# Kernel optimization log

Hardware: AMD Instinct MI355X
Metric: run time of the kernel (lower is better)

Reference implementation:

```python
import jax, jax.numpy as jnp
import numpy as np

BATCH, DIM, DB_SIZE, TOP_K = 2048, 512, 50000, 5

def setup_inputs() -> dict:
    key = jax.random.key(0)
    k1, k2 = jax.random.split(key)
    h_current = jax.random.normal(k1, (BATCH, DIM), dtype=jnp.float32)
    history_db = jax.random.normal(k2, (DB_SIZE, DIM), dtype=jnp.float32) * 0.01
    alpha = jnp.float32(0.5)
    return {"h_current": h_current, "history_db": history_db, "alpha": alpha, "top_k": TOP_K}

def _l2_normalize(x, eps=1e-12):
    # matches F.normalize(p=2): x / max(||x||, eps)
    n = jnp.linalg.norm(x, axis=-1, keepdims=True)
    return x / jnp.maximum(n, eps)

def reference(h_current, history_db, alpha, top_k):
    h_norm = _l2_normalize(h_current)            # (B, D)
    db_norm = _l2_normalize(history_db)          # (M, D)
    similarity = h_norm @ db_norm.T              # (B, M)
    topk_sim, topk_idx = jax.lax.top_k(similarity, top_k)  # (B, K)
    mu = jax.nn.softmax(topk_sim, axis=-1)       # (B, K)
    topk_embeddings = history_db[topk_idx]       # (B, K, D)
    h_retrieved = jnp.einsum('bk,bkd->bd', mu, topk_embeddings)
    a = jax.nn.sigmoid(alpha)
    return a * h_current + (1.0 - a) * h_retrieved
```

## Files before the change

### kernel.cpp

```cpp
#include <hip/hip_runtime.h>

#define BATCH   2048
#define DIM     512
#define DB_N    50000
#define TOPK    5
#define PADN    50176
#define NCHUNK  56
#define CTILES  7
#define CCOLS   896
#define TM      128
#define TN      128
#define NFIN    12

typedef float f32x4 __attribute__((ext_vector_type(4)));
typedef long long i64;

__device__ __forceinline__ void async16(const void* g, void* l) {
    __builtin_amdgcn_global_load_lds(
        (const __attribute__((address_space(1))) unsigned int*)g,
        (__attribute__((address_space(3))) unsigned int*)l, 16, 0, 0);
}

__device__ __forceinline__ unsigned sortbits(float v) {
    const int u = __float_as_int(v);
    return (unsigned)(u ^ ((u >> 31) | 0x80000000));
}

template<int NROWS>
__global__ void convert_kernel(const float* __restrict__ src, unsigned char* __restrict__ dst,
                               float* __restrict__ invp, int nreal) {
    const int r    = blockIdx.x * 4 + (threadIdx.x >> 6);
    const int lane = threadIdx.x & 63;
    float4 a = {0,0,0,0}, b = {0,0,0,0};
    float ss = 0.f;
    if (r < nreal) {
        const float* row = src + (size_t)r * DIM;
        a = *(const float4*)(row + lane * 8);
        b = *(const float4*)(row + lane * 8 + 4);
        ss = a.x*a.x + a.y*a.y + a.z*a.z + a.w*a.w
           + b.x*b.x + b.y*b.y + b.z*b.z + b.w*b.w;
    }
    #pragma unroll
    for (int off = 1; off < 64; off <<= 1) ss += __shfl_xor(ss, off);
    const float inv = 1.0f / fmaxf(sqrtf(ss), 1e-12f);
    const float s16 = inv * 16.0f;
    int lo = __builtin_amdgcn_cvt_pk_fp8_f32(a.x * s16, a.y * s16, 0, false);
    lo     = __builtin_amdgcn_cvt_pk_fp8_f32(a.z * s16, a.w * s16, lo, true);
    int hi = __builtin_amdgcn_cvt_pk_fp8_f32(b.x * s16, b.y * s16, 0, false);
    hi     = __builtin_amdgcn_cvt_pk_fp8_f32(b.z * s16, b.w * s16, hi, true);
    const int kb = lane >> 4;
    const int w  = (lane >> 1) & 7;
    int2 u2; u2.x = lo; u2.y = hi;
    *(int2*)(dst + ((size_t)kb * NROWS + r) * 128 + ((w ^ (r & 7)) << 4) + ((lane & 1) << 3)) = u2;
    if (invp && lane == 0) invp[r] = inv;
}

__global__ __launch_bounds__(512, 4) void sim_topk_kernel(
    const unsigned char* __restrict__ hzf, const unsigned char* __restrict__ dbzf,
    unsigned* __restrict__ pc) {

    __shared__ __align__(16) unsigned char As[2][TM * 128];
    __shared__ __align__(16) unsigned char Bs[2][TN * 128];
    __shared__ unsigned mrg[2][4][64][TOPK];

    const int tid  = threadIdx.x;
    const int lane = tid & 63;
    const int l15  = lane & 15;
    const int lhi  = lane >> 4;
    const int wid  = tid >> 6;
    const int uw   = __builtin_amdgcn_readfirstlane(wid);
    const int wm   = wid >> 2;
    const int wn   = wid & 3;
    const int mc   = blockIdx.x % NCHUNK;
    const int rb   = blockIdx.x / NCHUNK;
    const int c0   = mc * CCOLS;

    unsigned k0[16], k1[16];
    #pragma unroll
    for (int q = 0; q < 16; ++q) { k0[q] = 0u; k1[q] = 0u; }

    auto STAGE = [&](int buf, int t, int kb) {
        const unsigned char* ga = hzf +
            (((size_t)kb * BATCH + (size_t)rb * TM) * 8 + uw * 128 + lane) * 16;
        const unsigned char* gb = dbzf +
            (((size_t)kb * PADN + (size_t)(c0 + t * TN)) * 8 + uw * 128 + lane) * 16;
        async16(ga,        &As[buf][uw * 2048]);
        async16(ga + 1024, &As[buf][uw * 2048 + 1024]);
        async16(gb,        &Bs[buf][uw * 2048]);
        async16(gb + 1024, &Bs[buf][uw * 2048 + 1024]);
    };

    f32x4 acc[4][2];

    STAGE(0, 0, 0);

    int p = 0;
    #pragma unroll 1
    for (int t = 0; t < CTILES; ++t) {
        #pragma unroll
        for (int mf = 0; mf < 4; ++mf)
            #pragma unroll
            for (int nf = 0; nf < 2; ++nf) acc[mf][nf] = (f32x4){0.f, 0.f, 0.f, 0.f};

        #pragma unroll
        for (int kb = 0; kb < 4; ++kb) {
            const int np = p + 1;
            if (np < CTILES * 4) {
                STAGE(np & 1, np >> 2, np & 3);
                asm volatile("s_waitcnt vmcnt(4)" ::: "memory");
            } else {
                asm volatile("s_waitcnt vmcnt(0)" ::: "memory");
            }
            __builtin_amdgcn_s_barrier();
            __builtin_amdgcn_sched_barrier(0);

            const unsigned char* ta = As[p & 1];
            const unsigned char* tb = Bs[p & 1];
            #pragma unroll
            for (int ks = 0; ks < 4; ++ks) {
                const int sub = ks * 2 + (lhi >> 1);
                const int c8  = (lhi & 1) << 3;
                i64 af[4], bfr[2];
                #pragma unroll
                for (int mf = 0; mf < 4; ++mf) {
                    const int r = wm * 64 + mf * 16 + l15;
                    af[mf] = *(const i64*)(ta + r * 128 + ((sub ^ (r & 7)) << 4) + c8);
                }
                #pragma unroll
                for (int nf = 0; nf < 2; ++nf) {
                    const int r = wn * 32 + nf * 16 + l15;
                    bfr[nf] = *(const i64*)(tb + r * 128 + ((sub ^ (r & 7)) << 4) + c8);
                }
                __builtin_amdgcn_s_setprio(1);
                #pragma unroll
                for (int mf = 0; mf < 4; ++mf)
                    #pragma unroll
                    for (int nf = 0; nf < 2; ++nf)
                        acc[mf][nf] = __builtin_amdgcn_mfma_f32_16x16x32_fp8_fp8(
                            af[mf], bfr[nf], acc[mf][nf], 0, 0, 0);
                __builtin_amdgcn_s_setprio(0);
            }
            __builtin_amdgcn_sched_barrier(0);
            __builtin_amdgcn_s_barrier();
            ++p;
        }

        const int tc = c0 + t * TN;
        #pragma unroll
        for (int nf = 0; nf < 2; ++nf) {
            const int  gcol  = tc + wn * 32 + nf * 16 + l15;
            const bool valid = gcol < DB_N;
            #pragma unroll
            for (int mf = 0; mf < 4; ++mf)
                #pragma unroll
                for (int i = 0; i < 4; ++i) {
                    const int q = mf * 4 + i;
                    const unsigned key = valid
                        ? ((sortbits(acc[mf][nf][i]) & 0xFFFF0000u) | (unsigned)gcol) : 0u;
                    const unsigned hi2 = key > k0[q] ? key   : k0[q];
                    const unsigned lo2 = key > k0[q] ? k0[q] : key;
                    k1[q] = lo2 > k1[q] ? lo2 : k1[q];
                    k0[q] = hi2;
                }
        }
    }

    #pragma unroll
    for (int mf = 0; mf < 4; ++mf)
        #pragma unroll
        for (int i = 0; i < 4; ++i) {
            const int q = mf * 4 + i;
            unsigned a0 = k0[q], a1 = k1[q];
            #pragma unroll
            for (int it = 0; it < TOPK; ++it) {
                unsigned w = a0;
                #pragma unroll
                for (int sh = 1; sh < 16; sh <<= 1) {
                    const unsigned o = (unsigned)__shfl_xor((int)w, sh);
                    w = o > w ? o : w;
                }
                const bool own = (a0 == w) && (w != 0u);
                a0 = own ? a1 : a0;
                a1 = own ? 0u : a1;
                if (l15 == q) mrg[wm][wn][mf * 16 + lhi * 4 + i][it] = w;
            }
        }
    __syncthreads();

    if (wn == 0) {
        unsigned bv[TOPK] = {0u, 0u, 0u, 0u, 0u};
        #pragma unroll
        for (int qq = 0; qq < 4; ++qq)
            #pragma unroll
            for (int j = 0; j < TOPK; ++j) {
                const unsigned u = mrg[wm][qq][lane][j];
                #pragma unroll
                for (int k = TOPK - 1; k >= 1; --k) {
                    const bool gt  = u > bv[k];
                    const bool gtp = u > bv[k - 1];
                    bv[k] = gt ? (gtp ? bv[k - 1] : u) : bv[k];
                }
                if (u > bv[0]) bv[0] = u;
            }
        const int row = rb * TM + wm * 64 + lane;
        #pragma unroll
        for (int j = 0; j < TOPK; ++j)
            pc[((size_t)row * NCHUNK + mc) * TOPK + j] = bv[j];
    }
}

__global__ void finalize_kernel(const float* __restrict__ h, const float* __restrict__ db,
                                const float* __restrict__ alpha_p,
                                const unsigned* __restrict__ pc,
                                const float* __restrict__ inv_db,
                                float* __restrict__ out) {
    const int b    = blockIdx.x;
    const int tid  = threadIdx.x;
    const int lane = tid & 63;
    const int wv   = tid >> 6;
    const int NC   = NCHUNK * TOPK;

    __shared__ int   fid[NFIN];
    __shared__ float fsim[NFIN];
    __shared__ float invh_s;
    __shared__ float mu_s[TOPK];
    __shared__ int   id_s[TOPK];

    if (wv == 0) {
        const unsigned* cp = pc + (size_t)b * NC;
        unsigned v[5];
        #pragma unroll
        for (int j = 0; j < 5; ++j) {
            const int c = lane + j * 64;
            v[j] = (c < NC) ? cp[c] : 0u;
        }
        for (int it = 0; it < NFIN; ++it) {
            unsigned m = v[0];
            #pragma unroll
            for (int j = 1; j < 5; ++j) m = v[j] > m ? v[j] : m;
            #pragma unroll
            for (int sh = 1; sh < 64; sh <<= 1) {
                const unsigned o = (unsigned)__shfl_xor((int)m, sh);
                m = o > m ? o : m;
            }
            if (lane == 0) {
                int gi = (int)(m & 0xFFFFu);
                fid[it] = gi < DB_N ? gi : DB_N - 1;
            }
            #pragma unroll
            for (int j = 0; j < 5; ++j) if (v[j] == m) v[j] = 0u;
        }
    } else if (wv == 1) {
        const float* hr = h + (size_t)b * DIM;
        const float4 a = *(const float4*)(hr + lane * 8);
        const float4 c = *(const float4*)(hr + lane * 8 + 4);
        float ss = a.x*a.x + a.y*a.y + a.z*a.z + a.w*a.w
                 + c.x*c.x + c.y*c.y + c.z*c.z + c.w*c.w;
        #pragma unroll
        for (int off = 1; off < 64; off <<= 1) ss += __shfl_xor(ss, off);
        if (lane == 0) invh_s = 1.0f / fmaxf(sqrtf(ss), 1e-12f);
    }
    __syncthreads();

    const float* hr = h + (size_t)b * DIM;
    for (int f = wv; f < NFIN; f += 4) {
        const int gi = fid[f];
        const float* dr = db + (size_t)gi * DIM;
        const float4 ha = *(const float4*)(hr + lane * 8);
        const float4 hb = *(const float4*)(hr + lane * 8 + 4);
        const float4 da = *(const float4*)(dr + lane * 8);
        const float4 dc = *(const float4*)(dr + lane * 8 + 4);
        float d = ha.x*da.x + ha.y*da.y + ha.z*da.z + ha.w*da.w
                + hb.x*dc.x + hb.y*dc.y + hb.z*dc.z + hb.w*dc.w;
        #pragma unroll
        for (int off = 1; off < 64; off <<= 1) d += __shfl_xor(d, off);
        if (lane == 0) fsim[f] = d * invh_s * inv_db[gi];
    }
    __syncthreads();

    if (tid == 0) {
        bool used[NFIN];
        #pragma unroll
        for (int j = 0; j < NFIN; ++j) used[j] = false;
        float bv[TOPK]; int bi[TOPK];
        for (int it = 0; it < TOPK; ++it) {
            float m = -3.0e38f; int mj = 0, mi = 0x7fffffff;
            for (int j = 0; j < NFIN; ++j) {
                if (used[j]) continue;
                if (fsim[j] > m || (fsim[j] == m && fid[j] < mi)) {
                    m = fsim[j]; mj = j; mi = fid[j];
                }
            }
            used[mj] = true; bv[it] = m; bi[it] = mi;
        }
        float ssum = 0.f, w[TOPK];
        #pragma unroll
        for (int j = 0; j < TOPK; ++j) { w[j] = expf(bv[j] - bv[0]); ssum += w[j]; }
        #pragma unroll
        for (int j = 0; j < TOPK; ++j) { mu_s[j] = w[j] / ssum; id_s[j] = bi[j]; }
    }
    __syncthreads();

    const float a = 1.0f / (1.0f + expf(-alpha_p[0]));
    for (int d = tid; d < DIM; d += 256) {
        float r = 0.f;
        #pragma unroll
        for (int j = 0; j < TOPK; ++j) r += mu_s[j] * db[(size_t)id_s[j] * DIM + d];
        out[(size_t)b * DIM + d] = a * h[(size_t)b * DIM + d] + (1.f - a) * r;
    }
}

extern "C" void kernel_launch(void* const* d_in, const int* in_sizes, int n_in,
                              void* d_out, int out_size, void* d_ws, size_t ws_size,
                              hipStream_t stream) {
    const float* h     = (const float*)d_in[0];
    const float* db    = (const float*)d_in[1];
    const float* alpha = (const float*)d_in[2];
    float* out = (float*)d_out;

    const size_t dbzf_bytes = (size_t)PADN * DIM;
    const size_t hzf_bytes  = (size_t)BATCH * DIM;
    const size_t inv_bytes  = (size_t)PADN * 4;

    unsigned char* dbzf  = (unsigned char*)d_ws;
    unsigned char* hzf   = (unsigned char*)d_ws + dbzf_bytes;
    float*         invdb = (float*)((char*)d_ws + dbzf_bytes + hzf_bytes);
    unsigned*      pc    = (unsigned*)((char*)d_ws + dbzf_bytes + hzf_bytes + inv_bytes);

    convert_kernel<PADN><<<PADN / 4, 256, 0, stream>>>(db, dbzf, invdb, DB_N);
    convert_kernel<BATCH><<<BATCH / 4, 256, 0, stream>>>(h, hzf, nullptr, BATCH);
    sim_topk_kernel<<<16 * NCHUNK, 512, 0, stream>>>(hzf, dbzf, pc);
    finalize_kernel<<<BATCH, 256, 0, stream>>>(h, db, alpha, pc, invdb, out);
}
```

Measured before the change: 177.8 us.

## Enlarge similarity GEMM tile to 256x128 with triple-buffered LDS pipeline

Rewrites the fp8 similarity+top-k kernel to use 256x128 block tiles with 8 waves each computing a 64x64 sub-tile, and triple-buffers LDS loads two stages ahead instead of double buffering. MFMA work is split into four quadrant groups with explicit LDS fragment loads between them. Column chunks double (28 chunks of 1792 columns), halving the grid and the per-row partial candidate count that the finalize kernel scans. This raises arithmetic intensity and cuts redundant A/B traffic, at the cost of higher register and LDS use, occupancy limited to one block per CU, and only 224 blocks for 256 CUs.

New measurement: 192.9 us. 8.5% more time.

```diff
diff --git a/kernel.cpp b/kernel.cpp
--- a/kernel.cpp
+++ b/kernel.cpp
@@ -5,11 +5,12 @@
 #define DB_N    50000
 #define TOPK    5
 #define PADN    50176
-#define NCHUNK  56
-#define CTILES  7
-#define CCOLS   896
-#define TM      128
-#define TN      128
+#define NCHUNK  28
+#define CTILES  14
+#define CCOLS   1792
+#define KSTEPS  56
+#define BM      256
+#define BN      128
 #define NFIN    12
 
 typedef float f32x4 __attribute__((ext_vector_type(4)));
@@ -55,22 +56,21 @@
     if (invp && lane == 0) invp[r] = inv;
 }
 
-__global__ __launch_bounds__(512, 4) void sim_topk_kernel(
+__global__ __launch_bounds__(512, 1) void sim_topk_kernel(
     const unsigned char* __restrict__ hzf, const unsigned char* __restrict__ dbzf,
     unsigned* __restrict__ pc) {
 
-    __shared__ __align__(16) unsigned char As[2][TM * 128];
-    __shared__ __align__(16) unsigned char Bs[2][TN * 128];
-    __shared__ unsigned mrg[2][4][64][TOPK];
+    __shared__ __align__(16) unsigned char As[3][BM * 128];
+    __shared__ __align__(16) unsigned char Bs[3][BN * 128];
+    __shared__ unsigned mrg[4][2][64][TOPK];
 
     const int tid  = threadIdx.x;
     const int lane = tid & 63;
     const int l15  = lane & 15;
     const int lhi  = lane >> 4;
     const int wid  = tid >> 6;
-    const int uw   = __builtin_amdgcn_readfirstlane(wid);
-    const int wm   = wid >> 2;
-    const int wn   = wid & 3;
+    const int wm   = wid >> 1;
+    const int wn   = wid & 1;
     const int mc   = blockIdx.x % NCHUNK;
     const int rb   = blockIdx.x / NCHUNK;
     const int c0   = mc * CCOLS;
@@ -79,89 +79,146 @@
     #pragma unroll
     for (int q = 0; q < 16; ++q) { k0[q] = 0u; k1[q] = 0u; }
 
-    auto STAGE = [&](int buf, int t, int kb) {
-        const unsigned char* ga = hzf +
-            (((size_t)kb * BATCH + (size_t)rb * TM) * 8 + uw * 128 + lane) * 16;
-        const unsigned char* gb = dbzf +
-            (((size_t)kb * PADN + (size_t)(c0 + t * TN)) * 8 + uw * 128 + lane) * 16;
-        async16(ga,        &As[buf][uw * 2048]);
-        async16(ga + 1024, &As[buf][uw * 2048 + 1024]);
-        async16(gb,        &Bs[buf][uw * 2048]);
-        async16(gb + 1024, &Bs[buf][uw * 2048 + 1024]);
+    auto STAGE = [&](int s) {
+        const int buf = s % 3;
+        const int kb  = s & 3;
+        const int t   = s >> 2;
+        const unsigned char* ga = hzf + ((size_t)kb * BATCH + (size_t)rb * BM) * 128;
+        const unsigned char* gb = dbzf + ((size_t)kb * PADN + (size_t)(c0 + t * BN)) * 128;
+        #pragma unroll
+        for (int j = 0; j < 4; ++j)
+            async16(ga + tid * 16 + j * 8192, &As[buf][tid * 16 + j * 8192]);
+        #pragma unroll
+        for (int j = 0; j < 2; ++j)
+            async16(gb + tid * 16 + j * 8192, &Bs[buf][tid * 16 + j * 8192]);
     };
 
-    f32x4 acc[4][2];
-
-    STAGE(0, 0, 0);
-
-    int p = 0;
+    const int s2 = lhi >> 1;
+    const int c8 = (lhi & 1) << 3;
+
+    f32x4 acc[4][4];
+    #pragma unroll
+    for (int mf = 0; mf < 4; ++mf)
+        #pragma unroll
+        for (int nf = 0; nf < 4; ++nf) acc[mf][nf] = (f32x4){0.f, 0.f, 0.f, 0.f};
+
+    STAGE(0);
+    STAGE(1);
+
     #pragma unroll 1
-    for (int t = 0; t < CTILES; ++t) {
-        #pragma unroll
-        for (int mf = 0; mf < 4; ++mf)
-            #pragma unroll
-            for (int nf = 0; nf < 2; ++nf) acc[mf][nf] = (f32x4){0.f, 0.f, 0.f, 0.f};
-
-        #pragma unroll
-        for (int kb = 0; kb < 4; ++kb) {
-            const int np = p + 1;
-            if (np < CTILES * 4) {
-                STAGE(np & 1, np >> 2, np & 3);
-                asm volatile("s_waitcnt vmcnt(4)" ::: "memory");
-            } else {
-                asm volatile("s_waitcnt vmcnt(0)" ::: "memory");
-            }
-            __builtin_amdgcn_s_barrier();
-            __builtin_amdgcn_sched_barrier(0);
-
-            const unsigned char* ta = As[p & 1];
-            const unsigned char* tb = Bs[p & 1];
+    for (int s = 0; s < KSTEPS; ++s) {
+        if (s == KSTEPS - 1) { asm volatile("s_waitcnt vmcnt(0)" ::: "memory"); }
+        else                 { asm volatile("s_waitcnt vmcnt(6)" ::: "memory"); }
+        __builtin_amdgcn_s_barrier();
+        __builtin_amdgcn_sched_barrier(0);
+        if (s + 2 < KSTEPS) STAGE(s + 2);
+
+        const unsigned char* ta = As[s % 3];
+        const unsigned char* tb = Bs[s % 3];
+
+        i64 a0[8], a1[8], b0[8], b1[8];
+        #pragma unroll
+        for (int mf = 0; mf < 2; ++mf)
             #pragma unroll
             for (int ks = 0; ks < 4; ++ks) {
-                const int sub = ks * 2 + (lhi >> 1);
-                const int c8  = (lhi & 1) << 3;
-                i64 af[4], bfr[2];
-                #pragma unroll
-                for (int mf = 0; mf < 4; ++mf) {
-                    const int r = wm * 64 + mf * 16 + l15;
-                    af[mf] = *(const i64*)(ta + r * 128 + ((sub ^ (r & 7)) << 4) + c8);
-                }
-                #pragma unroll
-                for (int nf = 0; nf < 2; ++nf) {
-                    const int r = wn * 32 + nf * 16 + l15;
-                    bfr[nf] = *(const i64*)(tb + r * 128 + ((sub ^ (r & 7)) << 4) + c8);
-                }
-                __builtin_amdgcn_s_setprio(1);
+                const int r = wm * 64 + mf * 16 + l15;
+                a0[mf * 4 + ks] = *(const i64*)(ta + r * 128 + (((ks * 2 + s2) ^ (r & 7)) << 4) + c8);
+            }
+        #pragma unroll
+        for (int nf = 0; nf < 2; ++nf)
+            #pragma unroll
+            for (int ks = 0; ks < 4; ++ks) {
+                const int r = wn * 64 + nf * 16 + l15;
+                b0[nf * 4 + ks] = *(const i64*)(tb + r * 128 + (((ks * 2 + s2) ^ (r & 7)) << 4) + c8);
+            }
+        asm volatile("s_waitcnt lgkmcnt(0)" ::: "memory");
+        __builtin_amdgcn_sched_barrier(0);
+        __builtin_amdgcn_s_setprio(1);
+        #pragma unroll
+        for (int mf = 0; mf < 2; ++mf)
+            #pragma unroll
+            for (int nf = 0; nf < 2; ++nf)
+                #pragma unroll
+                for (int ks = 0; ks < 4; ++ks)
+                    acc[mf][nf] = __builtin_amdgcn_mfma_f32_16x16x32_fp8_fp8(
+                        a0[mf * 4 + ks], b0[nf * 4 + ks], acc[mf][nf], 0, 0, 0);
+        __builtin_amdgcn_s_setprio(0);
+        __builtin_amdgcn_sched_barrier(0);
+
+        #pragma unroll
+        for (int nf = 0; nf < 2; ++nf)
+            #pragma unroll
+            for (int ks = 0; ks < 4; ++ks) {
+                const int r = wn * 64 + (nf + 2) * 16 + l15;
+                b1[nf * 4 + ks] = *(const i64*)(tb + r * 128 + (((ks * 2 + s2) ^ (r & 7)) << 4) + c8);
+            }
+        asm volatile("s_waitcnt lgkmcnt(0)" ::: "memory");
+        __builtin_amdgcn_sched_barrier(0);
+        __builtin_amdgcn_s_setprio(1);
+        #pragma unroll
+        for (int mf = 0; mf < 2; ++mf)
+            #pragma unroll
+            for (int nf = 0; nf < 2; ++nf)
+                #pragma unroll
+                for (int ks = 0; ks < 4; ++ks)
+                    acc[mf][nf + 2] = __builtin_amdgcn_mfma_f32_16x16x32_fp8_fp8(
+                        a0[mf * 4 + ks], b1[nf * 4 + ks], acc[mf][nf + 2], 0, 0, 0);
+        __builtin_amdgcn_s_setprio(0);
+        __builtin_amdgcn_sched_barrier(0);
+
+        #pragma unroll
+        for (int mf = 0; mf < 2; ++mf)
+            #pragma unroll
+            for (int ks = 0; ks < 4; ++ks) {
+                const int r = wm * 64 + (mf + 2) * 16 + l15;
+                a1[mf * 4 + ks] = *(const i64*)(ta + r * 128 + (((ks * 2 + s2) ^ (r & 7)) << 4) + c8);
+            }
+        asm volatile("s_waitcnt lgkmcnt(0)" ::: "memory");
+        __builtin_amdgcn_sched_barrier(0);
+        __builtin_amdgcn_s_setprio(1);
+        #pragma unroll
+        for (int mf = 0; mf < 2; ++mf)
+            #pragma unroll
+            for (int nf = 0; nf < 2; ++nf)
+                #pragma unroll
+                for (int ks = 0; ks < 4; ++ks)
+                    acc[mf + 2][nf + 2] = __builtin_amdgcn_mfma_f32_16x16x32_fp8_fp8(
+                        a1[mf * 4 + ks], b1[nf * 4 + ks], acc[mf + 2][nf + 2], 0, 0, 0);
+        __builtin_amdgcn_s_setprio(0);
+        __builtin_amdgcn_sched_barrier(0);
+
+        __builtin_amdgcn_s_setprio(1);
+        #pragma unroll
+        for (int mf = 0; mf < 2; ++mf)
+            #pragma unroll
+            for (int nf = 0; nf < 2; ++nf)
+                #pragma unroll
+                for (int ks = 0; ks < 4; ++ks)
+                    acc[mf + 2][nf] = __builtin_amdgcn_mfma_f32_16x16x32_fp8_fp8(
+                        a1[mf * 4 + ks], b0[nf * 4 + ks], acc[mf + 2][nf], 0, 0, 0);
+        __builtin_amdgcn_s_setprio(0);
+        __builtin_amdgcn_sched_barrier(0);
+
+        if ((s & 3) == 3) {
+            const int tc = c0 + (s >> 2) * BN;
+            #pragma unroll
+            for (int nf = 0; nf < 4; ++nf) {
+                const int  gcol  = tc + wn * 64 + nf * 16 + l15;
+                const bool valid = gcol < DB_N;
                 #pragma unroll
                 for (int mf = 0; mf < 4; ++mf)
                     #pragma unroll
-                    for (int nf = 0; nf < 2; ++nf)
-                        acc[mf][nf] = __builtin_amdgcn_mfma_f32_16x16x32_fp8_fp8(
-                            af[mf], bfr[nf], acc[mf][nf], 0, 0, 0);
-                __builtin_amdgcn_s_setprio(0);
-            }
-            __builtin_amdgcn_sched_barrier(0);
-            __builtin_amdgcn_s_barrier();
-            ++p;
-        }
-
-        const int tc = c0 + t * TN;
-        #pragma unroll
-        for (int nf = 0; nf < 2; ++nf) {
-            const int  gcol  = tc + wn * 32 + nf * 16 + l15;
-            const bool valid = gcol < DB_N;
-            #pragma unroll
-            for (int mf = 0; mf < 4; ++mf)
-                #pragma unroll
-                for (int i = 0; i < 4; ++i) {
-                    const int q = mf * 4 + i;
-                    const unsigned key = valid
-                        ? ((sortbits(acc[mf][nf][i]) & 0xFFFF0000u) | (unsigned)gcol) : 0u;
-                    const unsigned hi2 = key > k0[q] ? key   : k0[q];
-                    const unsigned lo2 = key > k0[q] ? k0[q] : key;
-                    k1[q] = lo2 > k1[q] ? lo2 : k1[q];
-                    k0[q] = hi2;
-                }
+                    for (int i = 0; i < 4; ++i) {
+                        const int q = mf * 4 + i;
+                        const unsigned key = valid
+                            ? ((sortbits(acc[mf][nf][i]) & 0xFFFF0000u) | (unsigned)gcol) : 0u;
+                        const unsigned hi2 = key > k0[q] ? key   : k0[q];
+                        const unsigned lo2 = key > k0[q] ? k0[q] : key;
+                        k1[q] = lo2 > k1[q] ? lo2 : k1[q];
+                        k0[q] = hi2;
+                        acc[mf][nf][i] = 0.f;
+                    }
+            }
         }
     }
 
@@ -170,18 +227,18 @@
         #pragma unroll
         for (int i = 0; i < 4; ++i) {
             const int q = mf * 4 + i;
-            unsigned a0 = k0[q], a1 = k1[q];
+            unsigned a0k = k0[q], a1k = k1[q];
             #pragma unroll
             for (int it = 0; it < TOPK; ++it) {
-                unsigned w = a0;
+                unsigned w = a0k;
                 #pragma unroll
                 for (int sh = 1; sh < 16; sh <<= 1) {
                     const unsigned o = (unsigned)__shfl_xor((int)w, sh);
                     w = o > w ? o : w;
                 }
-                const bool own = (a0 == w) && (w != 0u);
-                a0 = own ? a1 : a0;
-                a1 = own ? 0u : a1;
+                const bool own = (a0k == w) && (w != 0u);
+                a0k = own ? a1k : a0k;
+                a1k = own ? 0u : a1k;
                 if (l15 == q) mrg[wm][wn][mf * 16 + lhi * 4 + i][it] = w;
             }
         }
@@ -190,7 +247,7 @@
     if (wn == 0) {
         unsigned bv[TOPK] = {0u, 0u, 0u, 0u, 0u};
         #pragma unroll
-        for (int qq = 0; qq < 4; ++qq)
+        for (int qq = 0; qq < 2; ++qq)
             #pragma unroll
             for (int j = 0; j < TOPK; ++j) {
                 const unsigned u = mrg[wm][qq][lane][j];
@@ -202,7 +259,7 @@
                 }
                 if (u > bv[0]) bv[0] = u;
             }
-        const int row = rb * TM + wm * 64 + lane;
+        const int row = rb * BM + wm * 64 + lane;
         #pragma unroll
         for (int j = 0; j < TOPK; ++j)
             pc[((size_t)row * NCHUNK + mc) * TOPK + j] = bv[j];
@@ -228,16 +285,16 @@
 
     if (wv == 0) {
         const unsigned* cp = pc + (size_t)b * NC;
-        unsigned v[5];
-        #pragma unroll
-        for (int j = 0; j < 5; ++j) {
+        unsigned v[3];
+        #pragma unroll
+        for (int j = 0; j < 3; ++j) {
             const int c = lane + j * 64;
             v[j] = (c < NC) ? cp[c] : 0u;
         }
         for (int it = 0; it < NFIN; ++it) {
             unsigned m = v[0];
             #pragma unroll
-            for (int j = 1; j < 5; ++j) m = v[j] > m ? v[j] : m;
+            for (int j = 1; j < 3; ++j) m = v[j] > m ? v[j] : m;
             #pragma unroll
             for (int sh = 1; sh < 64; sh <<= 1) {
                 const unsigned o = (unsigned)__shfl_xor((int)m, sh);
@@ -248,7 +305,7 @@
                 fid[it] = gi < DB_N ? gi : DB_N - 1;
             }
             #pragma unroll
-            for (int j = 0; j < 5; ++j) if (v[j] == m) v[j] = 0u;
+            for (int j = 0; j < 3; ++j) if (v[j] == m) v[j] = 0u;
         }
     } else if (wv == 1) {
         const float* hr = h + (size_t)b * DIM;
@@ -329,6 +386,6 @@
 
     convert_kernel<PADN><<<PADN / 4, 256, 0, stream>>>(db, dbzf, invdb, DB_N);
     convert_kernel<BATCH><<<BATCH / 4, 256, 0, stream>>>(h, hzf, nullptr, BATCH);
-    sim_topk_kernel<<<16 * NCHUNK, 512, 0, stream>>>(hzf, dbzf, pc);
+    sim_topk_kernel<<<8 * NCHUNK, 512, 0, stream>>>(hzf, dbzf, pc);
     finalize_kernel<<<BATCH, 256, 0, stream>>>(h, db, alpha, pc, invdb, out);
 }
```
